# Optimization experiments

Measured on AMD Instinct MI355X. Metric: run time of the kernel, lower is better.

The kernel has to match this reference:

```python
import jax, jax.numpy as jnp
import numpy as np

NEG = -10000.0
LN_EPS = 1e-5


def _longformer_attn(x, attn_val, Wq, bq, Wk, bk, Wv, bv, Wqg, bqg, Wkg, bkg, Wvg, bvg, w, H):
    # x: (B, S, D) with S % (2w) == 0; attn_val: (B, S) int, 0=local, -1=pad, +1=global (only last pos)
    B, S, D = x.shape
    d = D // H
    scale = float(1.0 / np.sqrt(d))
    q = (x @ Wq + bq).reshape(B, S, H, d) * scale
    k = (x @ Wk + bk).reshape(B, S, H, d)
    v = (x @ Wv + bv).reshape(B, S, H, d)
    g = S - 1                      # single global token (last position)
    C = S // w                     # number of query chunks of size w
    W3 = 3 * w
    # key/value windows: chunk c sees absolute keys [c*w - w, c*w + 2w)
    idx = np.arange(C)[:, None] * w + np.arange(W3)[None, :]           # (C, 3w) into padded length S+2w
    k_win = jnp.pad(k, ((0, 0), (w, w), (0, 0), (0, 0)))[:, idx]       # (B, C, 3w, H, d)
    v_win = jnp.pad(v, ((0, 0), (w, w), (0, 0), (0, 0)))[:, idx]
    qc = q.reshape(B, C, w, H, d)
    scores = jnp.einsum('bcxhd,bcyhd->bhcxy', qc, k_win)               # (B, H, C, w, 3w)
    # banded validity: relative offset in [-w, w] and absolute key index in [0, S)
    x_i = np.arange(w)[:, None]
    y_i = np.arange(W3)[None, :]
    rel_ok = (y_i - x_i >= 0) & (y_i - x_i <= 2 * w)                   # (w, 3w)
    j_abs = np.arange(C)[:, None, None] * w - w + y_i[None]            # (C, 1, 3w)
    valid = jnp.asarray(rel_ok[None] & ((j_abs >= 0) & (j_abs < S)))   # (C, w, 3w)
    # keys that are padding or global get -10000 inside the band (remove_from_windowed_attention_mask)
    rm_win = jnp.pad(attn_val != 0, ((0, 0), (w, w)))[:, idx]          # (B, C, 3w)
    scores = scores + jnp.where(rm_win, NEG, 0.0)[:, None, :, None, :]
    scores = jnp.where(valid[None, None], scores, -jnp.inf)
    # every query also attends to the global key (column prepended before softmax)
    g_scores = jnp.einsum('bcxhd,bhd->bhcx', qc, k[:, g])              # (B, H, C, w)
    all_s = jnp.concatenate([g_scores[..., None], scores], axis=-1)    # (B, H, C, w, 3w+1)
    probs = jax.nn.softmax(all_s, axis=-1)
    q_ok = (attn_val >= 0).astype(probs.dtype)                         # zero rows of padding queries
    probs = probs * q_ok.reshape(B, 1, C, w, 1)
    out = jnp.einsum('bhcxy,bcyhd->bcxhd', probs[..., 1:], v_win)
    out = out + jnp.einsum('bhcx,bhd->bcxhd', probs[..., 0], v[:, g])
    out = out.reshape(B, S, D)
    # global token: full attention over all keys with the *_global projections
    qg = (x[:, g] @ Wqg + bqg).reshape(B, H, d) * scale
    kg = (x @ Wkg + bkg).reshape(B, S, H, d)
    vg = (x @ Wvg + bvg).reshape(B, S, H, d)
    sg = jnp.einsum('bhd,bshd->bhs', qg, kg)
    sg = sg + jnp.where(attn_val < 0, NEG, 0.0)[:, None, :]
    og = jnp.einsum('bhs,bshd->bhd', jax.nn.softmax(sg, axis=-1), vg).reshape(B, D)
    return out.at[:, g].set(og)


def setup_inputs() -> dict:
    B, S, D, H, w, E = 2, 2048, 768, 12, 256, 4
    key = jax.random.key(0)
    ks = jax.random.split(key, 16)
    wmat = lambda k, s: jax.random.normal(k, s, dtype=jnp.float32) * 0.02
    inp = {
        'x': jax.random.normal(ks[0], (B, S, D), dtype=jnp.float32),
        'mask': jnp.ones((B, S), dtype=bool),
        'Wq': wmat(ks[1], (D, D)), 'bq': jnp.zeros((D,), jnp.float32),
        'Wk': wmat(ks[2], (D, D)), 'bk': jnp.zeros((D,), jnp.float32),
        'Wv': wmat(ks[3], (D, D)), 'bv': jnp.zeros((D,), jnp.float32),
        'Wqg': wmat(ks[4], (D, D)), 'bqg': jnp.zeros((D,), jnp.float32),
        'Wkg': wmat(ks[5], (D, D)), 'bkg': jnp.zeros((D,), jnp.float32),
        'Wvg': wmat(ks[6], (D, D)), 'bvg': jnp.zeros((D,), jnp.float32),
        'ln_g': jnp.ones((D,), jnp.float32), 'ln_b': jnp.zeros((D,), jnp.float32),
        'W1': wmat(ks[7], (D, E * D)), 'b1': jnp.zeros((E * D,), jnp.float32),
        'W2': wmat(ks[8], (E * D, D)), 'b2': jnp.zeros((D,), jnp.float32),
        'window_size': w,
        'num_heads': H,
    }
    return inp


def reference(x, mask, Wq, bq, Wk, bk, Wv, bv, Wqg, bqg, Wkg, bkg, Wvg, bvg,
              ln_g, ln_b, W1, b1, W2, b2, window_size, num_heads):
    B, S0, D = x.shape
    w = int(window_size)
    H = int(num_heads)
    pad = 2 * w - S0 % (2 * w)                          # always in [1, 2w], matches torch code
    xp = jnp.pad(x, ((0, 0), (0, pad), (0, 0)))         # pad_token_id = 0
    mp = jnp.pad(mask, ((0, 0), (0, pad)), constant_values=True)
    attn_val = mp.astype(jnp.int32) - 1                 # True->0 (local), False->-1 (pad)
    attn_val = attn_val.at[:, -1].set(1)                # last position is global
    xp = xp + _longformer_attn(xp, attn_val, Wq, bq, Wk, bk, Wv, bv,
                               Wqg, bqg, Wkg, bkg, Wvg, bvg, w, H)
    x1 = xp[:, :S0]
    mu = jnp.mean(x1, axis=-1, keepdims=True)
    var = jnp.mean((x1 - mu) ** 2, axis=-1, keepdims=True)
    xn = (x1 - mu) * jax.lax.rsqrt(var + LN_EPS) * ln_g + ln_b
    h = jax.nn.gelu(xn @ W1 + b1, approximate=False)
    return xn + h @ W2 + b2
```

## Files before the change

### kernel.cpp

```cpp
#include <hip/hip_runtime.h>
#include <hip/hip_bf16.h>

typedef unsigned short ushort_t;
typedef __attribute__((ext_vector_type(8))) __bf16 bf16x8;
typedef __attribute__((ext_vector_type(4))) float f32x4;
typedef __attribute__((ext_vector_type(4))) unsigned short us4;

#define S0 2048
#define DM 768
#define NH 12
#define DH 64
#define KS 2368
#define GK 2304

__device__ __forceinline__ float bf2f(ushort_t h){
  union{unsigned u; float f;} x; x.u = ((unsigned)h)<<16; return x.f;
}
__device__ __forceinline__ ushort_t f2bf(float f){
  union{float f; unsigned u;} x; x.f = f;
  unsigned r = (x.u + 0x7FFFu + ((x.u>>16)&1u))>>16;
  return (ushort_t)r;
}

typedef void as1_void __attribute__((address_space(1)));
typedef void as3_void __attribute__((address_space(3)));
__device__ __forceinline__ void lds_cp16(const void* g, void* s){
  __builtin_amdgcn_global_load_lds((as1_void*)g, (as3_void*)s, 16, 0, 0);
}

__device__ __forceinline__ int xcd_swizzle(int bid, int nwg){
  const int q8 = nwg>>3, r8 = nwg&7;
  const int xcd = bid & 7, sub = bid >> 3;
  return (xcd < r8 ? xcd*(q8+1) : r8*(q8+1) + (xcd-r8)*q8) + sub;
}

__global__ __launch_bounds__(256)
void prep_kernel(const float* __restrict__ Wq, const float* __restrict__ Wk,
                 const float* __restrict__ Wv, const float* __restrict__ W1,
                 const float* __restrict__ W2, const float* __restrict__ x,
                 const float* __restrict__ bq, const float* __restrict__ bk,
                 const float* __restrict__ bv,
                 ushort_t* __restrict__ WtQ, ushort_t* __restrict__ WtK,
                 ushort_t* __restrict__ WtV, ushort_t* __restrict__ Wt1,
                 ushort_t* __restrict__ Wt2, ushort_t* __restrict__ xb,
                 float* __restrict__ bqkv, ushort_t* __restrict__ Kb,
                 ushort_t* __restrict__ Vtb)
{
  __shared__ ushort_t tile[64][72];
  const int id = blockIdx.x, t = threadIdx.x;
  if (id < 1584){
    const float* src; ushort_t* dst; int K, N, bx, by;
    if (id < 432){
      const int m = id/144, r = id%144;
      src = (m==0)?Wq:((m==1)?Wk:Wv);
      dst = (m==0)?WtQ:((m==1)?WtK:WtV);
      K=768; N=768; bx=r%12; by=r/12;
    } else if (id < 1008){
      const int r = id-432; src=W1; dst=Wt1; K=768; N=3072; bx=r%48; by=r/48;
    } else {
      const int r = id-1008; src=W2; dst=Wt2; K=3072; N=768; bx=r%12; by=r/12;
    }
    const int n0 = bx*64, k0 = by*64;
    #pragma unroll
    for (int p=0; p<2; p++){
      int r = (t>>3) + p*32, c = (t&7)*8;
      const float* sp = src + (size_t)(k0+r)*N + n0 + c;
      const float4 a = *(const float4*)sp;
      const float4 b = *(const float4*)(sp+4);
      ushort_t v[8] = { f2bf(a.x), f2bf(a.y), f2bf(a.z), f2bf(a.w),
                        f2bf(b.x), f2bf(b.y), f2bf(b.z), f2bf(b.w) };
      *(int4*)&tile[r][c] = *(int4*)v;
    }
    __syncthreads();
    #pragma unroll
    for (int p=0; p<2; p++){
      int n = t&63, kc = (t>>6)*8 + p*32;
      ushort_t v[8];
      #pragma unroll
      for (int e=0; e<8; e++) v[e] = tile[kc+e][n];
      *(int4*)(dst + (size_t)(n0+n)*K + k0 + kc) = *(int4*)v;
    }
  } else if (id < 3120){
    const int i = (id-1584)*2048 + t*8;
    const float4 a = *(const float4*)(x+i);
    const float4 b = *(const float4*)(x+i+4);
    ushort_t v[8] = { f2bf(a.x), f2bf(a.y), f2bf(a.z), f2bf(a.w),
                      f2bf(b.x), f2bf(b.y), f2bf(b.z), f2bf(b.w) };
    *(int4*)(xb+i) = *(int4*)v;
  } else if (id < 3129){
    const int i = (id-3120)*256 + t;
    if (i < 2304)
      bqkv[i] = (i < 768) ? bq[i] : (i < 1536) ? bk[i-768] : bv[i-1536];
  } else if (id < 3369){
    const int i = (id-3129)*2048 + t*8;
    const int col = i % DM;
    const int rr  = i / DM;
    const int row = S0 + rr % (KS-S0);
    const int bb  = rr / (KS-S0);
    const float4 a = *(const float4*)(bk+col);
    const float4 b4 = *(const float4*)(bk+col+4);
    ushort_t v[8] = { f2bf(a.x), f2bf(a.y), f2bf(a.z), f2bf(a.w),
                      f2bf(b4.x), f2bf(b4.y), f2bf(b4.z), f2bf(b4.w) };
    *(int4*)&Kb[(size_t)bb*KS*DM + (size_t)row*DM + col] = *(int4*)v;
  } else {
    const int rid = id - 3369;
    const int h = (rid>>6) % NH;
    const int dd = rid & 63;
    const ushort_t val = f2bf(bv[h*64+dd]);
    if (t < 80){
      us4 pk = {val, val, val, val};
      *(us4*)&Vtb[(size_t)rid*KS + S0 + t*4] = pk;
    }
  }
}

template<int EPI, typename OT>
__global__ __launch_bounds__(256)
void gemm_bt(const ushort_t* __restrict__ A, const ushort_t* __restrict__ Bt,
             const float* __restrict__ bias, OT* __restrict__ C,
             const ushort_t* __restrict__ res,
             ushort_t* __restrict__ C2, ushort_t* __restrict__ C3,
             int K, int ldc, long long ldcb, int nbx)
{
  __shared__ ushort_t As[128*64];
  __shared__ ushort_t Bs[128*64];
  const int tid = threadIdx.x, wid = tid>>6, l = tid&63;

  const int wg = xcd_swizzle(blockIdx.x, gridDim.x);
  const int bx = wg % nbx, by = wg / nbx;
  const int m0 = by*128, n0 = bx*128;

  const int wm = wid>>1, wn = wid&1;
  const int lq = l&15, lg = l>>4;
  const int xa = lq&7;

  f32x4 acc[4][4];
  const f32x4 zero = {0.f,0.f,0.f,0.f};
  #pragma unroll
  for (int i=0;i<4;i++)
    #pragma unroll
    for (int j=0;j<4;j++) acc[i][j] = zero;

  const int swzc = ((l&7) ^ ((l>>3)&7)) * 8;
  const ushort_t* Ag = A  + (size_t)(m0 + wid*32 + (l>>3))*K + swzc;
  const ushort_t* Bg = Bt + (size_t)(n0 + wid*32 + (l>>3))*K + swzc;

  for (int k0=0; k0<K; k0+=64){
    #pragma unroll
    for (int i=0;i<4;i++){
      lds_cp16(Ag + (size_t)i*8*K + k0, As + wid*2048 + i*512);
      lds_cp16(Bg + (size_t)i*8*K + k0, Bs + wid*2048 + i*512);
    }
    __syncthreads();
    #pragma unroll
    for (int kk=0; kk<64; kk+=32){
      bf16x8 af[4], bfr[4];
      #pragma unroll
      for (int mi=0;mi<4;mi++)
        af[mi] = *(const bf16x8*)&As[(wm*64+mi*16+lq)*64 + ((((kk>>3)+lg)^xa)<<3)];
      #pragma unroll
      for (int ni=0;ni<4;ni++)
        bfr[ni] = *(const bf16x8*)&Bs[(wn*64+ni*16+lq)*64 + ((((kk>>3)+lg)^xa)<<3)];
      #pragma unroll
      for (int mi=0;mi<4;mi++)
        #pragma unroll
        for (int ni=0;ni<4;ni++)
          acc[mi][ni] = __builtin_amdgcn_mfma_f32_16x16x32_bf16(af[mi], bfr[ni], acc[mi][ni], 0,0,0);
    }
    __syncthreads();
  }

  if (EPI==4){
    const int seg = n0 / 768;
    if (seg == 2){
      #pragma unroll
      for (int mi=0;mi<4;mi++){
        const int mrow = m0 + wm*64 + mi*16 + lg*4;
        const int bb = mrow>>11, key = mrow&2047;
        #pragma unroll
        for (int ni=0;ni<4;ni++){
          const int ncol = n0 + wn*64 + ni*16 + lq;
          const int col = ncol - 1536;
          const float bvv = bias[ncol];
          us4 pk;
          #pragma unroll
          for (int r=0;r<4;r++) pk[r] = f2bf(acc[mi][ni][r] + bvv);
          *(us4*)&C3[((size_t)(bb*NH + (col>>6))*64 + (col&63))*KS + key] = pk;
        }
      }
      return;
    }
    ushort_t* dst = (seg==0) ? (ushort_t*)C : C2;
    const long long bstride = (seg==1) ? (long long)KS*DM : 2048LL*DM;
    const float sc = (seg==0) ? 0.125f : 1.f;
    #pragma unroll
    for (int mi=0;mi<4;mi++){
      const int mrow = m0 + wm*64 + mi*16 + lg*4;
      #pragma unroll
      for (int ni=0;ni<4;ni++){
        const int ncol = n0 + wn*64 + ni*16 + lq;
        const float bv = bias[ncol];
        const int col = ncol - seg*768;
        #pragma unroll
        for (int r=0;r<4;r++){
          const int m = mrow + r;
          const float v = (acc[mi][ni][r] + bv)*sc;
          dst[(size_t)((long long)(m>>11)*bstride) + (size_t)(m&2047)*DM + col] = f2bf(v);
        }
      }
    }
    return;
  }

  #pragma unroll
  for (int mi=0;mi<4;mi++){
    const int mrow = m0 + wm*64 + mi*16 + lg*4;
    #pragma unroll
    for (int ni=0;ni<4;ni++){
      const int ncol = n0 + wn*64 + ni*16 + lq;
      const float bv = bias[ncol];
      #pragma unroll
      for (int r=0;r<4;r++){
        const int m = mrow + r;
        float v = acc[mi][ni][r] + bv;
        if (EPI==2) v = 0.5f*v*(1.f + erff(v*0.70710678118f));
        if (EPI==3) v += bf2f(res[(size_t)m*ldc + ncol]);
        const size_t caddr = (size_t)((long long)(m>>11)*ldcb) + (size_t)(m&2047)*ldc + ncol;
        if constexpr (sizeof(OT)==4) C[caddr] = v;
        else                         C[caddr] = f2bf(v);
      }
    }
  }
}

__global__ __launch_bounds__(256)
void gemm64_bt(const ushort_t* __restrict__ A, const ushort_t* __restrict__ Bt,
               const float* __restrict__ bias, float* __restrict__ C,
               const ushort_t* __restrict__ res,
               int K, int ldc, int nbx)
{
  __shared__ ushort_t As[2][64*64];
  __shared__ ushort_t Bs[2][64*64];
  const int tid = threadIdx.x, wid = tid>>6, l = tid&63;

  const int wg = xcd_swizzle(blockIdx.x, gridDim.x);
  const int bx = wg % nbx, by = wg / nbx;
  const int m0 = by*64, n0 = bx*64;

  const int wm = wid>>1, wn = wid&1;
  const int lq = l&15, lg = l>>4;
  const int xa = lq&7;

  f32x4 acc[2][2];
  const f32x4 zero = {0.f,0.f,0.f,0.f};
  acc[0][0]=zero; acc[0][1]=zero; acc[1][0]=zero; acc[1][1]=zero;

  const int swzc = ((l&7) ^ ((l>>3)&7)) * 8;
  const ushort_t* Ag = A  + (size_t)(m0 + wid*16 + (l>>3))*K + swzc;
  const ushort_t* Bg = Bt + (size_t)(n0 + wid*16 + (l>>3))*K + swzc;

  const int nk = K>>6;

  #pragma unroll
  for (int i=0;i<2;i++){
    lds_cp16(Ag + (size_t)i*8*K, &As[0][wid*1024 + i*512]);
    lds_cp16(Bg + (size_t)i*8*K, &Bs[0][wid*1024 + i*512]);
  }
  __syncthreads();

  for (int t=0; t<nk; ++t){
    const int cur = t&1;
    if (t+1 < nk){
      const int k0 = (t+1)<<6;
      #pragma unroll
      for (int i=0;i<2;i++){
        lds_cp16(Ag + (size_t)i*8*K + k0, &As[cur^1][wid*1024 + i*512]);
        lds_cp16(Bg + (size_t)i*8*K + k0, &Bs[cur^1][wid*1024 + i*512]);
      }
    }
    #pragma unroll
    for (int kk=0; kk<64; kk+=32){
      bf16x8 af[2], bfr[2];
      #pragma unroll
      for (int mi=0;mi<2;mi++)
        af[mi] = *(const bf16x8*)&As[cur][(wm*32+mi*16+lq)*64 + ((((kk>>3)+lg)^xa)<<3)];
      #pragma unroll
      for (int ni=0;ni<2;ni++)
        bfr[ni] = *(const bf16x8*)&Bs[cur][(wn*32+ni*16+lq)*64 + ((((kk>>3)+lg)^xa)<<3)];
      #pragma unroll
      for (int mi=0;mi<2;mi++)
        #pragma unroll
        for (int ni=0;ni<2;ni++)
          acc[mi][ni] = __builtin_amdgcn_mfma_f32_16x16x32_bf16(af[mi], bfr[ni], acc[mi][ni], 0,0,0);
    }
    __syncthreads();
  }

  #pragma unroll
  for (int mi=0;mi<2;mi++){
    const int mrow = m0 + wm*32 + mi*16 + lg*4;
    #pragma unroll
    for (int ni=0;ni<2;ni++){
      const int ncol = n0 + wn*32 + ni*16 + lq;
      const float bv = bias[ncol];
      #pragma unroll
      for (int r=0;r<4;r++){
        const int m = mrow + r;
        float v = acc[mi][ni][r] + bv + bf2f(res[(size_t)m*ldc + ncol]);
        C[(size_t)m*ldc + ncol] = v;
      }
    }
  }
}

__global__ __launch_bounds__(512)
void attn_kernel(const ushort_t* __restrict__ Q, const ushort_t* __restrict__ Kw,
                 const ushort_t* __restrict__ Vt, const float* __restrict__ x,
                 ushort_t* __restrict__ xattn)
{
  __shared__ ushort_t Ks[2][64*64];
  __shared__ ushort_t Vs[2][64*64];
  __shared__ ushort_t P_lds[8][16][72];
  const int t = threadIdx.x, w = t>>6, l = t&63;
  const int qb = blockIdx.x, bh = blockIdx.y;
  const int b = bh/NH, h = bh%NH;
  const int qs = qb*128 + w*16;
  const int lq = l&15, lg = l>>4;
  const int i_q = qs + lq;
  const int kwin0 = qb*128 - 256;

  const int lo = w*16 - 63;
  const int cmin = lo > 0 ? ((lo+63)>>6) : 0;
  int cmax = (w*16 + 527) >> 6; if (cmax > 9) cmax = 9;

  const ushort_t* Qp = Q  + ((size_t)b*S0 + qs)*DM + h*DH;
  const ushort_t* Kp = Kw + (size_t)b*KS*DM + h*DH;
  const ushort_t* Vp = Vt + (size_t)bh*DH*KS;

  const bf16x8 qf0 = *(const bf16x8*)(Qp + (size_t)lq*DM + lg*8);
  const bf16x8 qf1 = *(const bf16x8*)(Qp + (size_t)lq*DM + 32 + lg*8);

  const int rl = l>>3;
  const int sslot = (l&7) ^ rl;

  const f32x4 zero = {0.f,0.f,0.f,0.f};
  f32x4 accO[4];
  #pragma unroll
  for (int g=0; g<4; g++) accO[g] = zero;
  float lsum = 0.f;

  auto stage = [&](int c, int bf){
    const int kbase = kwin0 + c*64;
    const int ck = w*8 + rl;
    int krow = kbase + ck; if (krow < 0) krow = 0;
    lds_cp16(Kp + (size_t)krow*DM + sslot*8, &Ks[bf][(w*8)*64]);
    int kcol = kbase + sslot*8; if (kcol < 0) kcol = 0;
    lds_cp16(Vp + (size_t)ck*KS + kcol,      &Vs[bf][(w*8)*64]);
  };

  stage(0, 0);
  for (int c=0; c<10; ++c){
    __syncthreads();
    if (c+1 < 10) stage(c+1, (c+1)&1);
    if (c >= cmin && c <= cmax){
      const int cur = c&1;
      const int kbase = kwin0 + c*64;
      const int slot0 = ((lg ^ (lq&7)) << 3);
      #pragma unroll
      for (int sb=0; sb<4; sb++){
        const bf16x8 kf0 = *(const bf16x8*)&Ks[cur][(sb*16+lq)*64 + slot0];
        const bf16x8 kf1 = *(const bf16x8*)&Ks[cur][(sb*16+lq)*64 + (slot0^32)];
        f32x4 s = zero;
        s = __builtin_amdgcn_mfma_f32_16x16x32_bf16(kf0, qf0, s, 0,0,0);
        s = __builtin_amdgcn_mfma_f32_16x16x32_bf16(kf1, qf1, s, 0,0,0);
        us4 pk;
        #pragma unroll
        for (int r=0; r<4; r++){
          const int j = kbase + sb*16 + lg*4 + r;
          const bool valid = (j >= 0) && (j < GK) && (j >= i_q-256) && (j <= i_q+256);
          const float p = valid ? __expf(s[r]) : 0.f;
          lsum += p;
          pk[r] = f2bf(p);
        }
        *(us4*)&P_lds[w][lq][sb*16 + lg*4] = pk;
      }
      #pragma unroll
      for (int r2=0; r2<2; r2++){
        const bf16x8 pf = *(const bf16x8*)&P_lds[w][lq][r2*32 + lg*8];
        #pragma unroll
        for (int g=0; g<4; g++){
          const int vslot = ((((r2<<2)|lg) ^ (lq&7)) << 3);
          const bf16x8 vtf = *(const bf16x8*)&Vs[cur][(g*16+lq)*64 + vslot];
          accO[g] = __builtin_amdgcn_mfma_f32_16x16x32_bf16(vtf, pf, accO[g], 0,0,0);
        }
      }
    }
  }

  {
    const ushort_t* kr = Kp + (size_t)(GK+lq)*DM + lg*8;
    const bf16x8 kf0 = *(const bf16x8*)(kr);
    const bf16x8 kf1 = *(const bf16x8*)(kr + 32);
    f32x4 s = zero;
    s = __builtin_amdgcn_mfma_f32_16x16x32_bf16(kf0, qf0, s, 0,0,0);
    s = __builtin_amdgcn_mfma_f32_16x16x32_bf16(kf1, qf1, s, 0,0,0);
    us4 pk, pz;
    #pragma unroll
    for (int r=0; r<4; r++){
      const float p = (lg==0 && r==0) ? __expf(s[r]) : 0.f;
      lsum += p;
      pk[r] = f2bf(p);
      pz[r] = 0;
    }
    *(us4*)&P_lds[w][lq][lg*4] = pk;
    *(us4*)&P_lds[w][lq][16 + lg*4] = pz;
    const bf16x8 pf = *(const bf16x8*)&P_lds[w][lq][lg*8];
    const int kb_lane = GK + (lg&1)*8;
    #pragma unroll
    for (int g=0; g<4; g++){
      const bf16x8 vtf = *(const bf16x8*)(Vp + (size_t)(g*16 + lq)*KS + kb_lane);
      accO[g] = __builtin_amdgcn_mfma_f32_16x16x32_bf16(vtf, pf, accO[g], 0,0,0);
    }
  }

  lsum += __shfl_xor(lsum, 16);
  lsum += __shfl_xor(lsum, 32);
  const float inv = 1.f / lsum;

  const float* xr = x + ((size_t)b*S0 + i_q)*DM + h*DH;
  ushort_t* outp = xattn + ((size_t)b*S0 + i_q)*DM + h*DH;
  #pragma unroll
  for (int g=0; g<4; g++){
    const float4 xv = *(const float4*)(xr + g*16 + lg*4);
    us4 o;
    o[0] = f2bf(accO[g][0]*inv + xv.x);
    o[1] = f2bf(accO[g][1]*inv + xv.y);
    o[2] = f2bf(accO[g][2]*inv + xv.z);
    o[3] = f2bf(accO[g][3]*inv + xv.w);
    *(us4*)(outp + g*16 + lg*4) = o;
  }
}

__global__ __launch_bounds__(192)
void ln_kernel(const ushort_t* __restrict__ xattn, const float* __restrict__ gam,
               const float* __restrict__ bet, ushort_t* __restrict__ xn)
{
  const int row = blockIdx.x, t = threadIdx.x;
  const us4 xv = *(const us4*)(xattn + (size_t)row*DM + t*4);
  float v[4];
  float s = 0.f, ss = 0.f;
  #pragma unroll
  for (int r=0;r<4;r++){ v[r] = bf2f(xv[r]); s += v[r]; ss += v[r]*v[r]; }
  #pragma unroll
  for (int o=1; o<64; o<<=1){ s += __shfl_xor(s,o); ss += __shfl_xor(ss,o); }
  __shared__ float red[3][2];
  if ((t&63)==0){ red[t>>6][0]=s; red[t>>6][1]=ss; }
  __syncthreads();
  const float S  = red[0][0]+red[1][0]+red[2][0];
  const float SS = red[0][1]+red[1][1]+red[2][1];
  const float mu = S*(1.f/768.f);
  const float var = SS*(1.f/768.f) - mu*mu;
  const float rs = rsqrtf(var + 1e-5f);
  const float4 g4 = *(const float4*)(gam + t*4);
  const float4 b4 = *(const float4*)(bet + t*4);
  us4 o;
  o[0] = f2bf((v[0]-mu)*rs*g4.x + b4.x);
  o[1] = f2bf((v[1]-mu)*rs*g4.y + b4.y);
  o[2] = f2bf((v[2]-mu)*rs*g4.z + b4.z);
  o[3] = f2bf((v[3]-mu)*rs*g4.w + b4.w);
  *(us4*)(xn + (size_t)row*DM + t*4) = o;
}

extern "C" void kernel_launch(void* const* d_in, const int* in_sizes, int n_in,
                              void* d_out, int out_size, void* d_ws, size_t ws_size,
                              hipStream_t stream)
{
  const float* x   = (const float*)d_in[0];
  const float* Wq  = (const float*)d_in[2];
  const float* bq  = (const float*)d_in[3];
  const float* Wk  = (const float*)d_in[4];
  const float* bk  = (const float*)d_in[5];
  const float* Wv  = (const float*)d_in[6];
  const float* bv  = (const float*)d_in[7];
  const float* lng = (const float*)d_in[14];
  const float* lnb = (const float*)d_in[15];
  const float* W1  = (const float*)d_in[16];
  const float* b1  = (const float*)d_in[17];
  const float* W2  = (const float*)d_in[18];
  const float* b2  = (const float*)d_in[19];
  float* out = (float*)d_out;

  char* ws = (char*)d_ws;
  ushort_t* xb  = (ushort_t*)(ws + 0);
  ushort_t* Qb  = (ushort_t*)(ws + 6291456);
  ushort_t* Kb  = (ushort_t*)(ws + 12582912);
  ushort_t* Vtb = (ushort_t*)(ws + 19857408);
  ushort_t* hb  = (ushort_t*)(ws + 0);
  size_t o2 = 27131904;
  ushort_t* WtQ = (ushort_t*)(ws + o2); o2 += 1179648;
  ushort_t* WtK = (ushort_t*)(ws + o2); o2 += 1179648;
  ushort_t* WtV = (ushort_t*)(ws + o2); o2 += 1179648;
  ushort_t* Wt1 = (ushort_t*)(ws + o2); o2 += 4718592;
  ushort_t* Wt2 = (ushort_t*)(ws + o2); o2 += 4718592;
  ushort_t* xat = (ushort_t*)(ws + o2); o2 += 6291456;
  ushort_t* xnb = (ushort_t*)(ws + o2); o2 += 6291456;
  float*    bqkv= (float*)   (ws + o2); o2 += 9216;
  (void)ws_size; (void)in_sizes; (void)n_in; (void)out_size;

  prep_kernel<<<4905,256,0,stream>>>(Wq, Wk, Wv, W1, W2, x, bq, bk, bv,
                                     WtQ, WtK, WtV, Wt1, Wt2, xb, bqkv, Kb, Vtb);

  gemm_bt<4,ushort_t><<<576,256,0,stream>>>(xb, WtQ, bqkv, Qb, nullptr, Kb, Vtb,
                                            768, 768, 0LL, 18);

  attn_kernel<<<dim3(16,24),512,0,stream>>>(Qb, Kb, Vtb, x, xat);

  ln_kernel<<<4096,192,0,stream>>>(xat, lng, lnb, xnb);

  gemm_bt<2,ushort_t><<<768,256,0,stream>>>(xnb, Wt1, b1, hb, nullptr, nullptr, nullptr,
                                            768, 3072, 2048LL*3072, 24);
  gemm64_bt<<<768,256,0,stream>>>(hb, Wt2, b2, out, xnb, 3072, 768, 12);
}
```

Measured before the change: 153.7 us.

## Narrow GEMM N-tile to 96, single-buffer attention LDS, fast-path full-valid chunks

The GEMM template gains an NF parameter, and both the QKV and FFN1 GEMMs now use 128x96 tiles, which launches more workgroups across the CUs. The unused residual and fp32 epilogue paths are removed. The attention kernel drops LDS double buffering in favour of a single buffer with an extra barrier per chunk, and adds a launch-bounds occupancy hint. It also skips per-element mask checks for chunks that are entirely valid and packs the probabilities with v_cvt_pk_bf16_f32. The trade-off is lost load/compute overlap in attention in exchange for lower LDS use and possibly higher occupancy, plus smaller GEMM tiles that reuse data less.

```diff
diff --git a/kernel.cpp b/kernel.cpp
--- a/kernel.cpp
+++ b/kernel.cpp
@@ -114,57 +114,57 @@
   }
 }
 
-template<int EPI, typename OT>
+template<int EPI, int NF, typename OT>
 __global__ __launch_bounds__(256)
 void gemm_bt(const ushort_t* __restrict__ A, const ushort_t* __restrict__ Bt,
              const float* __restrict__ bias, OT* __restrict__ C,
-             const ushort_t* __restrict__ res,
              ushort_t* __restrict__ C2, ushort_t* __restrict__ C3,
              int K, int ldc, long long ldcb, int nbx)
 {
   __shared__ ushort_t As[128*64];
-  __shared__ ushort_t Bs[128*64];
+  __shared__ ushort_t Bs[NF*32*64];
   const int tid = threadIdx.x, wid = tid>>6, l = tid&63;
 
   const int wg = xcd_swizzle(blockIdx.x, gridDim.x);
   const int bx = wg % nbx, by = wg / nbx;
-  const int m0 = by*128, n0 = bx*128;
+  const int m0 = by*128, n0 = bx*(NF*32);
 
   const int wm = wid>>1, wn = wid&1;
   const int lq = l&15, lg = l>>4;
   const int xa = lq&7;
 
-  f32x4 acc[4][4];
+  f32x4 acc[4][NF];
   const f32x4 zero = {0.f,0.f,0.f,0.f};
   #pragma unroll
   for (int i=0;i<4;i++)
     #pragma unroll
-    for (int j=0;j<4;j++) acc[i][j] = zero;
+    for (int j=0;j<NF;j++) acc[i][j] = zero;
 
   const int swzc = ((l&7) ^ ((l>>3)&7)) * 8;
   const ushort_t* Ag = A  + (size_t)(m0 + wid*32 + (l>>3))*K + swzc;
-  const ushort_t* Bg = Bt + (size_t)(n0 + wid*32 + (l>>3))*K + swzc;
+  const ushort_t* Bg = Bt + (size_t)(n0 + wid*(NF*8) + (l>>3))*K + swzc;
 
   for (int k0=0; k0<K; k0+=64){
     #pragma unroll
-    for (int i=0;i<4;i++){
+    for (int i=0;i<4;i++)
       lds_cp16(Ag + (size_t)i*8*K + k0, As + wid*2048 + i*512);
-      lds_cp16(Bg + (size_t)i*8*K + k0, Bs + wid*2048 + i*512);
-    }
+    #pragma unroll
+    for (int i=0;i<NF;i++)
+      lds_cp16(Bg + (size_t)i*8*K + k0, Bs + wid*(NF*512) + i*512);
     __syncthreads();
     #pragma unroll
     for (int kk=0; kk<64; kk+=32){
-      bf16x8 af[4], bfr[4];
+      bf16x8 af[4], bfr[NF];
       #pragma unroll
       for (int mi=0;mi<4;mi++)
         af[mi] = *(const bf16x8*)&As[(wm*64+mi*16+lq)*64 + ((((kk>>3)+lg)^xa)<<3)];
       #pragma unroll
-      for (int ni=0;ni<4;ni++)
-        bfr[ni] = *(const bf16x8*)&Bs[(wn*64+ni*16+lq)*64 + ((((kk>>3)+lg)^xa)<<3)];
+      for (int ni=0;ni<NF;ni++)
+        bfr[ni] = *(const bf16x8*)&Bs[(wn*(NF*16)+ni*16+lq)*64 + ((((kk>>3)+lg)^xa)<<3)];
       #pragma unroll
       for (int mi=0;mi<4;mi++)
         #pragma unroll
-        for (int ni=0;ni<4;ni++)
+        for (int ni=0;ni<NF;ni++)
           acc[mi][ni] = __builtin_amdgcn_mfma_f32_16x16x32_bf16(af[mi], bfr[ni], acc[mi][ni], 0,0,0);
     }
     __syncthreads();
@@ -178,8 +178,8 @@
         const int mrow = m0 + wm*64 + mi*16 + lg*4;
         const int bb = mrow>>11, key = mrow&2047;
         #pragma unroll
-        for (int ni=0;ni<4;ni++){
-          const int ncol = n0 + wn*64 + ni*16 + lq;
+        for (int ni=0;ni<NF;ni++){
+          const int ncol = n0 + wn*(NF*16) + ni*16 + lq;
           const int col = ncol - 1536;
           const float bvv = bias[ncol];
           us4 pk;
@@ -197,8 +197,8 @@
     for (int mi=0;mi<4;mi++){
       const int mrow = m0 + wm*64 + mi*16 + lg*4;
       #pragma unroll
-      for (int ni=0;ni<4;ni++){
-        const int ncol = n0 + wn*64 + ni*16 + lq;
+      for (int ni=0;ni<NF;ni++){
+        const int ncol = n0 + wn*(NF*16) + ni*16 + lq;
         const float bv = bias[ncol];
         const int col = ncol - seg*768;
         #pragma unroll
@@ -216,18 +216,16 @@
   for (int mi=0;mi<4;mi++){
     const int mrow = m0 + wm*64 + mi*16 + lg*4;
     #pragma unroll
-    for (int ni=0;ni<4;ni++){
-      const int ncol = n0 + wn*64 + ni*16 + lq;
+    for (int ni=0;ni<NF;ni++){
+      const int ncol = n0 + wn*(NF*16) + ni*16 + lq;
       const float bv = bias[ncol];
       #pragma unroll
       for (int r=0;r<4;r++){
         const int m = mrow + r;
         float v = acc[mi][ni][r] + bv;
         if (EPI==2) v = 0.5f*v*(1.f + erff(v*0.70710678118f));
-        if (EPI==3) v += bf2f(res[(size_t)m*ldc + ncol]);
         const size_t caddr = (size_t)((long long)(m>>11)*ldcb) + (size_t)(m&2047)*ldc + ncol;
-        if constexpr (sizeof(OT)==4) C[caddr] = v;
-        else                         C[caddr] = f2bf(v);
+        C[caddr] = f2bf(v);
       }
     }
   }
@@ -313,13 +311,13 @@
   }
 }
 
-__global__ __launch_bounds__(512)
+__global__ __launch_bounds__(512, 6)
 void attn_kernel(const ushort_t* __restrict__ Q, const ushort_t* __restrict__ Kw,
                  const ushort_t* __restrict__ Vt, const float* __restrict__ x,
                  ushort_t* __restrict__ xattn)
 {
-  __shared__ ushort_t Ks[2][64*64];
-  __shared__ ushort_t Vs[2][64*64];
+  __shared__ ushort_t Ks[64*64];
+  __shared__ ushort_t Vs[64*64];
   __shared__ ushort_t P_lds[8][16][72];
   const int t = threadIdx.x, w = t>>6, l = t&63;
   const int qb = blockIdx.x, bh = blockIdx.y;
@@ -349,40 +347,48 @@
   for (int g=0; g<4; g++) accO[g] = zero;
   float lsum = 0.f;
 
-  auto stage = [&](int c, int bf){
+  auto stage = [&](int c){
     const int kbase = kwin0 + c*64;
     const int ck = w*8 + rl;
     int krow = kbase + ck; if (krow < 0) krow = 0;
-    lds_cp16(Kp + (size_t)krow*DM + sslot*8, &Ks[bf][(w*8)*64]);
+    lds_cp16(Kp + (size_t)krow*DM + sslot*8, &Ks[(w*8)*64]);
     int kcol = kbase + sslot*8; if (kcol < 0) kcol = 0;
-    lds_cp16(Vp + (size_t)ck*KS + kcol,      &Vs[bf][(w*8)*64]);
+    lds_cp16(Vp + (size_t)ck*KS + kcol,      &Vs[(w*8)*64]);
   };
 
-  stage(0, 0);
+  stage(0);
+  __syncthreads();
   for (int c=0; c<10; ++c){
-    __syncthreads();
-    if (c+1 < 10) stage(c+1, (c+1)&1);
     if (c >= cmin && c <= cmax){
-      const int cur = c&1;
       const int kbase = kwin0 + c*64;
+      const bool fullv = (kbase >= 0) && (kbase + 63 < GK) &&
+                         (kbase >= qs - 241) && (kbase <= qs + 193);
       const int slot0 = ((lg ^ (lq&7)) << 3);
       #pragma unroll
       for (int sb=0; sb<4; sb++){
-        const bf16x8 kf0 = *(const bf16x8*)&Ks[cur][(sb*16+lq)*64 + slot0];
-        const bf16x8 kf1 = *(const bf16x8*)&Ks[cur][(sb*16+lq)*64 + (slot0^32)];
+        const bf16x8 kf0 = *(const bf16x8*)&Ks[(sb*16+lq)*64 + slot0];
+        const bf16x8 kf1 = *(const bf16x8*)&Ks[(sb*16+lq)*64 + (slot0^32)];
         f32x4 s = zero;
         s = __builtin_amdgcn_mfma_f32_16x16x32_bf16(kf0, qf0, s, 0,0,0);
         s = __builtin_amdgcn_mfma_f32_16x16x32_bf16(kf1, qf1, s, 0,0,0);
-        us4 pk;
-        #pragma unroll
-        for (int r=0; r<4; r++){
-          const int j = kbase + sb*16 + lg*4 + r;
-          const bool valid = (j >= 0) && (j < GK) && (j >= i_q-256) && (j <= i_q+256);
-          const float p = valid ? __expf(s[r]) : 0.f;
-          lsum += p;
-          pk[r] = f2bf(p);
+        float pv[4];
+        if (fullv){
+          #pragma unroll
+          for (int r=0; r<4; r++) pv[r] = __expf(s[r]);
+        } else {
+          #pragma unroll
+          for (int r=0; r<4; r++){
+            const int j = kbase + sb*16 + lg*4 + r;
+            const bool valid = (j >= 0) && (j < GK) && (j >= i_q-256) && (j <= i_q+256);
+            pv[r] = valid ? __expf(s[r]) : 0.f;
+          }
         }
-        *(us4*)&P_lds[w][lq][sb*16 + lg*4] = pk;
+        lsum += (pv[0]+pv[1]) + (pv[2]+pv[3]);
+        unsigned a0, a1;
+        asm("v_cvt_pk_bf16_f32 %0, %1, %2" : "=v"(a0) : "v"(pv[0]), "v"(pv[1]));
+        asm("v_cvt_pk_bf16_f32 %0, %1, %2" : "=v"(a1) : "v"(pv[2]), "v"(pv[3]));
+        uint2 pk2; pk2.x = a0; pk2.y = a1;
+        *(uint2*)&P_lds[w][lq][sb*16 + lg*4] = pk2;
       }
       #pragma unroll
       for (int r2=0; r2<2; r2++){
@@ -390,10 +396,15 @@
         #pragma unroll
         for (int g=0; g<4; g++){
           const int vslot = ((((r2<<2)|lg) ^ (lq&7)) << 3);
-          const bf16x8 vtf = *(const bf16x8*)&Vs[cur][(g*16+lq)*64 + vslot];
+          const bf16x8 vtf = *(const bf16x8*)&Vs[(g*16+lq)*64 + vslot];
           accO[g] = __builtin_amdgcn_mfma_f32_16x16x32_bf16(vtf, pf, accO[g], 0,0,0);
         }
       }
+    }
+    __syncthreads();
+    if (c+1 < 10){
+      stage(c+1);
+      __syncthreads();
     }
   }
 
@@ -510,14 +521,14 @@
   prep_kernel<<<4905,256,0,stream>>>(Wq, Wk, Wv, W1, W2, x, bq, bk, bv,
                                      WtQ, WtK, WtV, Wt1, Wt2, xb, bqkv, Kb, Vtb);
 
-  gemm_bt<4,ushort_t><<<576,256,0,stream>>>(xb, WtQ, bqkv, Qb, nullptr, Kb, Vtb,
-                                            768, 768, 0LL, 18);
+  gemm_bt<4,3,ushort_t><<<768,256,0,stream>>>(xb, WtQ, bqkv, Qb, Kb, Vtb,
+                                              768, 768, 0LL, 24);
 
   attn_kernel<<<dim3(16,24),512,0,stream>>>(Qb, Kb, Vtb, x, xat);
 
   ln_kernel<<<4096,192,0,stream>>>(xat, lng, lnb, xnb);
 
-  gemm_bt<2,ushort_t><<<768,256,0,stream>>>(xnb, Wt1, b1, hb, nullptr, nullptr, nullptr,
-                                            768, 3072, 2048LL*3072, 24);
+  gemm_bt<2,3,ushort_t><<<1024,256,0,stream>>>(xnb, Wt1, b1, hb, nullptr, nullptr,
+                                               768, 3072, 2048LL*3072, 32);
   gemm64_bt<<<768,256,0,stream>>>(hb, Wt2, b2, out, xnb, 3072, 768, 12);
 }
```

Result: faster. 137.4 us (-10.6%).
